# Kernel optimization log

Measured on AMD Instinct MI355X. Metric: run time of the kernel, lower is better.

## Reference

```python
import jax, jax.numpy as jnp
import numpy as np

B, L, ENC, DEC, HID = 256, 196, 2048, 512, 512


def setup_inputs() -> dict:
    key = jax.random.key(0)
    ks = jax.random.split(key, 8)
    s_enc = 1.0 / np.sqrt(ENC)
    s_dec = 1.0 / np.sqrt(DEC)
    s_hid = 1.0 / np.sqrt(HID)
    return {
        "feature": jax.random.normal(ks[0], (B, L, ENC), dtype=jnp.float32),
        "hidden": jax.random.normal(ks[1], (B, DEC), dtype=jnp.float32),
        # nn.Linear params (PyTorch default uniform init ranges)
        "Wf": jax.random.uniform(ks[2], (HID, ENC), jnp.float32, -s_enc, s_enc),
        "bf": jax.random.uniform(ks[3], (HID,), jnp.float32, -s_enc, s_enc),
        "Wh": jax.random.uniform(ks[4], (HID, DEC), jnp.float32, -s_dec, s_dec),
        "bh": jax.random.uniform(ks[5], (HID,), jnp.float32, -s_dec, s_dec),
        "We": jax.random.uniform(ks[6], (1, HID), jnp.float32, -s_hid, s_hid),
        "be": jax.random.uniform(ks[7], (1,), jnp.float32, -s_hid, s_hid),
    }


def reference(feature, hidden, Wf, bf, Wh, bh, We, be):
    # feature: [B, L, ENC], hidden: [B, DEC]
    feat_emb = jnp.einsum("ble,he->blh", feature, Wf) + bf          # [B, L, HID]
    hid_emb = (hidden @ Wh.T + bh)[:, None, :]                        # [B, 1, HID]
    emb = jax.nn.relu(feat_emb + hid_emb)                             # [B, L, HID]
    score = jnp.einsum("blh,h->bl", emb, We[0]) + be[0]               # [B, L]
    weight = jax.nn.softmax(score, axis=1)                            # [B, L]
    output = jnp.einsum("bl,ble->be", weight, feature)                # [B, ENC]
    return (output, weight)
```

## Files before the change

### kernel.cpp

```cpp
#include <hip/hip_runtime.h>
#include <hip/hip_bf16.h>
#include <math.h>

#define B_   256
#define L_   196
#define ENC_ 2048
#define DEC_ 512
#define HID_ 512

typedef __attribute__((ext_vector_type(8))) short short8v;
typedef __attribute__((ext_vector_type(4))) short short4v;
typedef __attribute__((ext_vector_type(4))) float f32x4;

static __device__ __forceinline__ short f2bf(float x) {
    unsigned u = __float_as_uint(x);
    u += 0x7fffu + ((u >> 16) & 1u);
    return (short)(u >> 16);
}

__global__ __launch_bounds__(256) void kconvert(const float* __restrict__ Wf,
                                                short* __restrict__ wfbf) {
    int idx = (blockIdx.x * 256 + threadIdx.x) * 4;
    int n  = idx >> 11;
    int e0 = idx & 2047;
    float4 f = *(const float4*)(Wf + idx);
    short4v h;
    h.x = f2bf(f.x); h.y = f2bf(f.y); h.z = f2bf(f.z); h.w = f2bf(f.w);
    int unit = (e0 >> 3) ^ (n & 7);
    int off  = n * 2048 + unit * 8 + (e0 & 7);
    *(short4v*)(wfbf + off) = h;
}

__global__ __launch_bounds__(512) void khid(const float* __restrict__ hidden,
                                            const float* __restrict__ Wh,
                                            const float* __restrict__ bh,
                                            float* __restrict__ hid_emb) {
    __shared__ float hs[8][512];
    int t = threadIdx.x;
    int bg = blockIdx.x * 8;
    #pragma unroll
    for (int i = 0; i < 8; ++i) hs[i][t] = hidden[(size_t)(bg + i) * 512 + t];
    __syncthreads();
    float acc[8] = {0.f,0.f,0.f,0.f,0.f,0.f,0.f,0.f};
    const float4* wrow = (const float4*)(Wh + (size_t)t * 512);
    #pragma unroll 4
    for (int d4 = 0; d4 < 128; ++d4) {
        float4 w = wrow[d4];
        int d = d4 * 4;
        #pragma unroll
        for (int i = 0; i < 8; ++i)
            acc[i] += w.x * hs[i][d] + w.y * hs[i][d+1] + w.z * hs[i][d+2] + w.w * hs[i][d+3];
    }
    float bhv = bh[t];
    #pragma unroll
    for (int i = 0; i < 8; ++i)
        hid_emb[(size_t)(bg + i) * 512 + t] = acc[i] + bhv;
}

__global__ __launch_bounds__(512, 2) void kscore(
    const float* __restrict__ feat, const short* __restrict__ wfbf,
    const float* __restrict__ bf, const float* __restrict__ hid_emb,
    const float* __restrict__ We, const float* __restrict__ be,
    float* __restrict__ score)
{
    __shared__ short lds_b[2 * 512 * 64];
    __shared__ short lds_a[2 * 64 * 64];
    __shared__ float score_s[8][64];

    const int tid  = threadIdx.x;
    const int wave = tid >> 6;
    const int lane = tid & 63;
    const int g    = lane >> 4;
    const int c    = lane & 15;
    const int m0   = blockIdx.x * 64;

    const int ch0 = tid,       r0 = ch0 >> 4, c40 = ch0 & 15;
    const int ch1 = tid + 512, r1 = ch1 >> 4, c41 = ch1 & 15;
    const float* gA0 = feat + (size_t)(m0 + r0) * ENC_ + c40 * 4;
    const float* gA1 = feat + (size_t)(m0 + r1) * ENC_ + c41 * 4;
    const int boff0 = r0 * 128 + (((c40 >> 1) ^ (r0 & 7)) << 4) + (c40 & 1) * 8;
    const int boff1 = r1 * 128 + (((c41 >> 1) ^ (r1 & 7)) << 4) + (c41 & 1) * 8;

    f32x4 acc[4][4];
    #pragma unroll
    for (int i = 0; i < 4; ++i)
        #pragma unroll
        for (int j = 0; j < 4; ++j)
            acc[i][j] = (f32x4)0.f;

#define STAGE_B(K0, BUF)                                                      \
    {                                                                         \
        short* bbase = lds_b + (size_t)(BUF) * 32768;                         \
        _Pragma("unroll")                                                     \
        for (int j = 0; j < 8; ++j) {                                         \
            int ubase = j * 512 + wave * 64;                                  \
            int ulin  = ubase + lane;                                         \
            int n = ulin >> 3, u = ulin & 7;                                  \
            const short* gp = wfbf + (size_t)n * ENC_ + (K0) + u * 8;         \
            short* lp = bbase + (size_t)ubase * 8;                            \
            __builtin_amdgcn_global_load_lds(                                 \
                (const __attribute__((address_space(1))) void*)gp,            \
                (__attribute__((address_space(3))) void*)lp, 16, 0, 0);       \
        }                                                                     \
    }

#define COMPUTE_TILE(BUF)                                                     \
    {                                                                         \
        const char* la = (const char*)lds_a + (BUF) * 8192;                   \
        const char* lb = (const char*)lds_b + (BUF) * 65536;                  \
        _Pragma("unroll")                                                     \
        for (int kf = 0; kf < 2; ++kf) {                                      \
            short8v af[4], bq[4];                                             \
            _Pragma("unroll")                                                 \
            for (int mi = 0; mi < 4; ++mi) {                                  \
                int row = mi * 16 + c;                                        \
                int un  = (kf * 4 + g) ^ (row & 7);                           \
                af[mi] = *(const short8v*)(la + row * 128 + un * 16);         \
            }                                                                 \
            _Pragma("unroll")                                                 \
            for (int ni = 0; ni < 4; ++ni) {                                  \
                int n  = wave * 64 + ni * 16 + c;                             \
                int un = (kf * 4 + g) ^ (n & 7);                              \
                bq[ni] = *(const short8v*)(lb + n * 128 + un * 16);           \
            }                                                                 \
            _Pragma("unroll")                                                 \
            for (int mi = 0; mi < 4; ++mi)                                    \
                _Pragma("unroll")                                             \
                for (int ni = 0; ni < 4; ++ni)                                \
                    acc[mi][ni] = __builtin_amdgcn_mfma_f32_16x16x32_bf16(    \
                        af[mi], bq[ni], acc[mi][ni], 0, 0, 0);                \
        }                                                                     \
    }

#define WRITE_A(FA, FB, BUF)                                                  \
    {                                                                         \
        short4v h0, h1;                                                       \
        h0.x = f2bf((FA).x); h0.y = f2bf((FA).y);                             \
        h0.z = f2bf((FA).z); h0.w = f2bf((FA).w);                             \
        h1.x = f2bf((FB).x); h1.y = f2bf((FB).y);                             \
        h1.z = f2bf((FB).z); h1.w = f2bf((FB).w);                             \
        char* wa = (char*)lds_a + (BUF) * 8192;                               \
        *(short4v*)(wa + boff0) = h0;                                         \
        *(short4v*)(wa + boff1) = h1;                                         \
    }

#define BAR_COUNTED(N)                                                        \
    asm volatile("s_waitcnt vmcnt(" #N ") lgkmcnt(0)" ::: "memory");          \
    __builtin_amdgcn_sched_barrier(0);                                        \
    __builtin_amdgcn_s_barrier();                                             \
    __builtin_amdgcn_sched_barrier(0);

    float4 fa_cur0 = *(const float4*)(gA0);
    float4 fa_cur1 = *(const float4*)(gA1);
    STAGE_B(0, 0)
    float4 fa_nxt0 = *(const float4*)(gA0 + 64);
    float4 fa_nxt1 = *(const float4*)(gA1 + 64);
    WRITE_A(fa_cur0, fa_cur1, 0)
    fa_cur0 = fa_nxt0; fa_cur1 = fa_nxt1;
    BAR_COUNTED(2)

    for (int kt = 0; kt < 30; ++kt) {
        const int pcur = kt & 1;
        const int kb = (kt + 1) * 64;
        const int ka = (kt + 2) * 64;
        STAGE_B(kb, pcur ^ 1)
        fa_nxt0 = *(const float4*)(gA0 + ka);
        fa_nxt1 = *(const float4*)(gA1 + ka);
        COMPUTE_TILE(pcur)
        WRITE_A(fa_cur0, fa_cur1, pcur ^ 1)
        fa_cur0 = fa_nxt0; fa_cur1 = fa_nxt1;
        BAR_COUNTED(2)
    }
    STAGE_B(31 * 64, 1)
    COMPUTE_TILE(0)
    WRITE_A(fa_cur0, fa_cur1, 1)
    BAR_COUNTED(0)
    COMPUTE_TILE(1)

#undef STAGE_B
#undef COMPUTE_TILE
#undef WRITE_A
#undef BAR_COUNTED

    float wev[4], bfv[4];
    #pragma unroll
    for (int ni = 0; ni < 4; ++ni) {
        int n = wave * 64 + ni * 16 + c;
        wev[ni] = We[n];
        bfv[ni] = bf[n];
    }
    #pragma unroll
    for (int mi = 0; mi < 4; ++mi) {
        float part[4] = {0.f, 0.f, 0.f, 0.f};
        #pragma unroll
        for (int j = 0; j < 4; ++j) {
            int row  = mi * 16 + g * 4 + j;
            int bidx = (m0 + row) / 196;
            const float* hrow = hid_emb + (size_t)bidx * 512;
            #pragma unroll
            for (int ni = 0; ni < 4; ++ni) {
                int n = wave * 64 + ni * 16 + c;
                float v = acc[mi][ni][j] + bfv[ni] + hrow[n];
                v = fmaxf(v, 0.f);
                part[j] += v * wev[ni];
            }
        }
        #pragma unroll
        for (int j = 0; j < 4; ++j) {
            float p = part[j];
            p += __shfl_xor(p, 1, 16);
            p += __shfl_xor(p, 2, 16);
            p += __shfl_xor(p, 4, 16);
            p += __shfl_xor(p, 8, 16);
            if (c == 0) score_s[wave][mi * 16 + g * 4 + j] = p;
        }
    }
    __syncthreads();
    if (tid < 64) {
        float s = be[0];
        #pragma unroll
        for (int w = 0; w < 8; ++w) s += score_s[w][tid];
        score[m0 + tid] = s;
    }
}

__global__ __launch_bounds__(256) void kout(
    const float* __restrict__ score, const float* __restrict__ feat,
    float* __restrict__ out_o, float* __restrict__ out_w)
{
    __shared__ float wbuf[196];
    __shared__ float red[8];
    int t    = threadIdx.x;
    int b    = blockIdx.x >> 1;
    int half = blockIdx.x & 1;
    int w    = t >> 6, lane = t & 63;

    float s = (t < 196) ? score[b * 196 + t] : -1e30f;
    float m = s;
    #pragma unroll
    for (int off = 32; off >= 1; off >>= 1) m = fmaxf(m, __shfl_xor(m, off, 64));
    if (lane == 0) red[w] = m;
    __syncthreads();
    m = fmaxf(fmaxf(red[0], red[1]), fmaxf(red[2], red[3]));
    float e = (t < 196) ? __expf(s - m) : 0.f;
    float sum = e;
    #pragma unroll
    for (int off = 32; off >= 1; off >>= 1) sum += __shfl_xor(sum, off, 64);
    if (lane == 0) red[4 + w] = sum;
    __syncthreads();
    sum = red[4] + red[5] + red[6] + red[7];
    float wt = e / sum;
    if (t < 196) {
        wbuf[t] = wt;
        if (half == 0) out_w[b * 196 + t] = wt;
    }
    __syncthreads();

    int e0 = half * 1024 + t * 4;
    float4 acc = make_float4(0.f, 0.f, 0.f, 0.f);
    const float* fb = feat + (size_t)b * L_ * ENC_ + e0;
    #pragma unroll 4
    for (int l = 0; l < 196; ++l) {
        float4 v = *(const float4*)(fb + (size_t)l * ENC_);
        float wl = wbuf[l];
        acc.x += wl * v.x; acc.y += wl * v.y; acc.z += wl * v.z; acc.w += wl * v.w;
    }
    *(float4*)(out_o + (size_t)b * ENC_ + e0) = acc;
}

extern "C" void kernel_launch(void* const* d_in, const int* in_sizes, int n_in,
                              void* d_out, int out_size, void* d_ws, size_t ws_size,
                              hipStream_t stream) {
    (void)in_sizes; (void)n_in; (void)out_size; (void)ws_size;
    const float* feature = (const float*)d_in[0];
    const float* hidden  = (const float*)d_in[1];
    const float* Wf      = (const float*)d_in[2];
    const float* bf      = (const float*)d_in[3];
    const float* Wh      = (const float*)d_in[4];
    const float* bh      = (const float*)d_in[5];
    const float* We      = (const float*)d_in[6];
    const float* be      = (const float*)d_in[7];

    char* ws = (char*)d_ws;
    short* wfbf    = (short*)ws;
    float* hid_emb = (float*)(ws + (2u << 20));
    float* score   = (float*)(ws + (2u << 20) + (512u << 10));

    float* out_o = (float*)d_out;
    float* out_w = out_o + (size_t)B_ * ENC_;

    kconvert<<<dim3(1024), dim3(256), 0, stream>>>(Wf, wfbf);
    khid<<<dim3(32), dim3(512), 0, stream>>>(hidden, Wh, bh, hid_emb);
    kscore<<<dim3(784), dim3(512), 0, stream>>>(feature, wfbf, bf, hid_emb, We, be, score);
    kout<<<dim3(512), dim3(256), 0, stream>>>(score, feature, (float*)d_out, out_w);
}
```

Before: 323.3 us.

## Halve K-tile to 32 to cut LDS and raise kscore occupancy

Shrinks the K-step of the fused score GEMM from 64 to 32, halving the LDS buffers for A and B. Launch bounds go from 2 to 4 blocks per CU. The bf16 weight pre-layout and the LDS swizzle change to a 4-unit XOR pattern that matches the new 64-byte rows. The aim is more resident waves to hide global-load latency, at the cost of twice as many barriers and K iterations, and tighter register limits that could spill the accumulators.

```diff
diff --git a/kernel.cpp b/kernel.cpp
--- a/kernel.cpp
+++ b/kernel.cpp
@@ -26,8 +26,10 @@
     float4 f = *(const float4*)(Wf + idx);
     short4v h;
     h.x = f2bf(f.x); h.y = f2bf(f.y); h.z = f2bf(f.z); h.w = f2bf(f.w);
-    int unit = (e0 >> 3) ^ (n & 7);
-    int off  = n * 2048 + unit * 8 + (e0 & 7);
+    int tile = e0 >> 5;
+    int lu   = (e0 >> 3) & 3;
+    int pu   = lu ^ ((n >> 1) & 3);
+    int off  = n * 2048 + tile * 32 + pu * 8 + (e0 & 7);
     *(short4v*)(wfbf + off) = h;
 }
 
@@ -57,14 +59,14 @@
         hid_emb[(size_t)(bg + i) * 512 + t] = acc[i] + bhv;
 }
 
-__global__ __launch_bounds__(512, 2) void kscore(
+__global__ __launch_bounds__(512, 4) void kscore(
     const float* __restrict__ feat, const short* __restrict__ wfbf,
     const float* __restrict__ bf, const float* __restrict__ hid_emb,
     const float* __restrict__ We, const float* __restrict__ be,
     float* __restrict__ score)
 {
-    __shared__ short lds_b[2 * 512 * 64];
-    __shared__ short lds_a[2 * 64 * 64];
+    __shared__ short lds_b[2 * 512 * 32];
+    __shared__ short lds_a[2 * 64 * 32];
     __shared__ float score_s[8][64];
 
     const int tid  = threadIdx.x;
@@ -74,12 +76,10 @@
     const int c    = lane & 15;
     const int m0   = blockIdx.x * 64;
 
-    const int ch0 = tid,       r0 = ch0 >> 4, c40 = ch0 & 15;
-    const int ch1 = tid + 512, r1 = ch1 >> 4, c41 = ch1 & 15;
-    const float* gA0 = feat + (size_t)(m0 + r0) * ENC_ + c40 * 4;
-    const float* gA1 = feat + (size_t)(m0 + r1) * ENC_ + c41 * 4;
-    const int boff0 = r0 * 128 + (((c40 >> 1) ^ (r0 & 7)) << 4) + (c40 & 1) * 8;
-    const int boff1 = r1 * 128 + (((c41 >> 1) ^ (r1 & 7)) << 4) + (c41 & 1) * 8;
+    const int r_a  = tid >> 3;
+    const int c4   = tid & 7;
+    const float* gA = feat + (size_t)(m0 + r_a) * ENC_ + c4 * 4;
+    const int boffA = r_a * 64 + (((c4 >> 1) ^ ((r_a >> 1) & 3)) << 4) + (c4 & 1) * 8;
 
     f32x4 acc[4][4];
     #pragma unroll
@@ -90,12 +90,12 @@
 
 #define STAGE_B(K0, BUF)                                                      \
     {                                                                         \
-        short* bbase = lds_b + (size_t)(BUF) * 32768;                         \
-        _Pragma("unroll")                                                     \
-        for (int j = 0; j < 8; ++j) {                                         \
-            int ubase = j * 512 + wave * 64;                                  \
-            int ulin  = ubase + lane;                                         \
-            int n = ulin >> 3, u = ulin & 7;                                  \
+        short* bbase = lds_b + (size_t)(BUF) * 16384;                         \
+        _Pragma("unroll")                                                     \
+        for (int j = 0; j < 4; ++j) {                                         \
+            int ubase = j * 512 + wave * 64;       \
+            int ulin  = ubase + lane;              \
+            int n = ulin >> 2, u = ulin & 3;                                  \
             const short* gp = wfbf + (size_t)n * ENC_ + (K0) + u * 8;         \
             short* lp = bbase + (size_t)ubase * 8;                            \
             __builtin_amdgcn_global_load_lds(                                 \
@@ -106,42 +106,36 @@
 
 #define COMPUTE_TILE(BUF)                                                     \
     {                                                                         \
-        const char* la = (const char*)lds_a + (BUF) * 8192;                   \
-        const char* lb = (const char*)lds_b + (BUF) * 65536;                  \
-        _Pragma("unroll")                                                     \
-        for (int kf = 0; kf < 2; ++kf) {                                      \
-            short8v af[4], bq[4];                                             \
+        const char* la = (const char*)lds_a + (BUF) * 4096;                   \
+        const char* lb = (const char*)lds_b + (BUF) * 32768;                  \
+        short8v af[4], bq[4];                                                 \
+        _Pragma("unroll")                                                     \
+        for (int mi = 0; mi < 4; ++mi) {                                      \
+            int row = mi * 16 + c;                                            \
+            int un  = g ^ ((row >> 1) & 3);                                   \
+            af[mi] = *(const short8v*)(la + row * 64 + un * 16);              \
+        }                                                                     \
+        _Pragma("unroll")                                                     \
+        for (int ni = 0; ni < 4; ++ni) {                                      \
+            int n  = wave * 64 + ni * 16 + c;                                 \
+            int un = g ^ ((n >> 1) & 3);                                      \
+            bq[ni] = *(const short8v*)(lb + n * 64 + un * 16);                \
+        }                                                                     \
+        _Pragma("unroll")                                                     \
+        for (int mi = 0; mi < 4; ++mi)                                        \
             _Pragma("unroll")                                                 \
-            for (int mi = 0; mi < 4; ++mi) {                                  \
-                int row = mi * 16 + c;                                        \
-                int un  = (kf * 4 + g) ^ (row & 7);                           \
-                af[mi] = *(const short8v*)(la + row * 128 + un * 16);         \
-            }                                                                 \
-            _Pragma("unroll")                                                 \
-            for (int ni = 0; ni < 4; ++ni) {                                  \
-                int n  = wave * 64 + ni * 16 + c;                             \
-                int un = (kf * 4 + g) ^ (n & 7);                              \
-                bq[ni] = *(const short8v*)(lb + n * 128 + un * 16);           \
-            }                                                                 \
-            _Pragma("unroll")                                                 \
-            for (int mi = 0; mi < 4; ++mi)                                    \
-                _Pragma("unroll")                                             \
-                for (int ni = 0; ni < 4; ++ni)                                \
-                    acc[mi][ni] = __builtin_amdgcn_mfma_f32_16x16x32_bf16(    \
-                        af[mi], bq[ni], acc[mi][ni], 0, 0, 0);                \
-        }                                                                     \
-    }
-
-#define WRITE_A(FA, FB, BUF)                                                  \
+            for (int ni = 0; ni < 4; ++ni)                                    \
+                acc[mi][ni] = __builtin_amdgcn_mfma_f32_16x16x32_bf16(        \
+                    af[mi], bq[ni], acc[mi][ni], 0, 0, 0);                    \
+    }
+
+#define WRITE_A(FA, BUF)                                                      \
     {                                                                         \
-        short4v h0, h1;                                                       \
+        short4v h0;                                                           \
         h0.x = f2bf((FA).x); h0.y = f2bf((FA).y);                             \
         h0.z = f2bf((FA).z); h0.w = f2bf((FA).w);                             \
-        h1.x = f2bf((FB).x); h1.y = f2bf((FB).y);                             \
-        h1.z = f2bf((FB).z); h1.w = f2bf((FB).w);                             \
-        char* wa = (char*)lds_a + (BUF) * 8192;                               \
-        *(short4v*)(wa + boff0) = h0;                                         \
-        *(short4v*)(wa + boff1) = h1;                                         \
+        char* wa = (char*)lds_a + (BUF) * 4096;                               \
+        *(short4v*)(wa + boffA) = h0;                                         \
     }
 
 #define BAR_COUNTED(N)                                                        \
@@ -150,30 +144,25 @@
     __builtin_amdgcn_s_barrier();                                             \
     __builtin_amdgcn_sched_barrier(0);
 
-    float4 fa_cur0 = *(const float4*)(gA0);
-    float4 fa_cur1 = *(const float4*)(gA1);
+    float4 fa_cur = *(const float4*)(gA);
     STAGE_B(0, 0)
-    float4 fa_nxt0 = *(const float4*)(gA0 + 64);
-    float4 fa_nxt1 = *(const float4*)(gA1 + 64);
-    WRITE_A(fa_cur0, fa_cur1, 0)
-    fa_cur0 = fa_nxt0; fa_cur1 = fa_nxt1;
-    BAR_COUNTED(2)
-
-    for (int kt = 0; kt < 30; ++kt) {
+    float4 fa_nxt = *(const float4*)(gA + 32);
+    WRITE_A(fa_cur, 0)
+    fa_cur = fa_nxt;
+    BAR_COUNTED(1)
+
+    for (int kt = 0; kt < 62; ++kt) {
         const int pcur = kt & 1;
-        const int kb = (kt + 1) * 64;
-        const int ka = (kt + 2) * 64;
-        STAGE_B(kb, pcur ^ 1)
-        fa_nxt0 = *(const float4*)(gA0 + ka);
-        fa_nxt1 = *(const float4*)(gA1 + ka);
+        STAGE_B((kt + 1) * 32, pcur ^ 1)
+        fa_nxt = *(const float4*)(gA + (kt + 2) * 32);
         COMPUTE_TILE(pcur)
-        WRITE_A(fa_cur0, fa_cur1, pcur ^ 1)
-        fa_cur0 = fa_nxt0; fa_cur1 = fa_nxt1;
-        BAR_COUNTED(2)
-    }
-    STAGE_B(31 * 64, 1)
+        WRITE_A(fa_cur, pcur ^ 1)
+        fa_cur = fa_nxt;
+        BAR_COUNTED(1)
+    }
+    STAGE_B(63 * 32, 1)
     COMPUTE_TILE(0)
-    WRITE_A(fa_cur0, fa_cur1, 1)
+    WRITE_A(fa_cur, 1)
     BAR_COUNTED(0)
     COMPUTE_TILE(1)
 
```

After: 318.8 us. About the same (-1.4%).
